# Kernel optimization log

Measured on AMD Instinct MI355X. Metric: run time of the kernel, lower is better.

The kernel has to match this reference:

```python
import jax, jax.numpy as jnp
import numpy as np

D_EMBD = 1024
N_HEADS = 16
D_HEAD = D_EMBD // N_HEADS
BS, T = 2, 2048


def setup_inputs() -> dict:
    key = jax.random.key(0)
    ks = jax.random.split(key, 5)
    s1 = 1.0 / np.sqrt(D_EMBD)
    x = jax.random.normal(ks[0], (BS, T, D_EMBD), dtype=jnp.float32)
    # dense1: Linear(d_embd, 3*d_embd); stored as [in, out] matmul matrix
    W1 = jax.random.uniform(ks[1], (D_EMBD, 3 * D_EMBD), jnp.float32, -s1, s1)
    b1 = jax.random.uniform(ks[2], (3 * D_EMBD,), jnp.float32, -s1, s1)
    # dense2: Linear(d_embd, d_embd)
    W2 = jax.random.uniform(ks[3], (D_EMBD, D_EMBD), jnp.float32, -s1, s1)
    b2 = jax.random.uniform(ks[4], (D_EMBD,), jnp.float32, -s1, s1)
    return {"x": x, "W1": W1, "b1": b1, "W2": W2, "b2": b2}


def reference(x, W1, b1, W2, b2):
    bs, t, d = x.shape
    kqv = x @ W1 + b1                               # [b, t, 3d]
    # torch.chunk order in source: k, q, v
    k, q, v = jnp.split(kqv, 3, axis=-1)
    def heads(z):  # [b, t, (h d)] -> [b, h, t, d]
        return z.reshape(bs, t, N_HEADS, D_HEAD).transpose(0, 2, 1, 3)
    k, q, v = heads(k), heads(q), heads(v)
    scale = 1.0 / np.sqrt(D_HEAD).astype(np.float32)
    attn = jnp.einsum('bhtd,bhsd->bhts', q, k) * scale   # [b, h, t, t]
    causal = jnp.tril(jnp.ones((t, t), dtype=bool))
    attn = jnp.where(causal, attn, -jnp.inf)
    attn = jax.nn.softmax(attn, axis=-1)
    out = jnp.einsum('bhts,bhsd->bhtd', attn, v)         # [b, h, t, d]
    out = out.transpose(0, 2, 1, 3).reshape(bs, t, d)    # [b, t, (h d)]
    return out @ W2 + b2
```

## Files before the change

### kernel.cpp

```cpp
#include <hip/hip_runtime.h>

typedef unsigned short ushort_t;
typedef short bf16x8 __attribute__((ext_vector_type(8)));
typedef float f32x4 __attribute__((ext_vector_type(4)));

__device__ __forceinline__ unsigned f2bf(float f) {
    union { float f; unsigned u; } c; c.f = f;
    unsigned u = c.u;
    u += 0x7FFFu + ((u >> 16) & 1u);
    return u >> 16;
}

__device__ __forceinline__ void async16(const ushort_t* g, ushort_t* l) {
    __builtin_amdgcn_global_load_lds(
        (const __attribute__((address_space(1))) unsigned int*)g,
        (__attribute__((address_space(3))) unsigned int*)l, 16, 0, 0);
}

__global__ __launch_bounds__(256) void prep_kernel(
    const float* __restrict__ x, const float* __restrict__ W1, const float* __restrict__ W2,
    ushort_t* __restrict__ xb, ushort_t* __restrict__ w1t, ushort_t* __restrict__ w2t) {
    __shared__ float tile[64][65];
    const int tid = threadIdx.x;
    const int bid = blockIdx.x;
    if (bid < 2048) {
        const int i = (bid * 256 + tid) * 8;
        const float4 a = *(const float4*)(x + i);
        const float4 b = *(const float4*)(x + i + 4);
        uint4 pk;
        pk.x = f2bf(a.x) | (f2bf(a.y) << 16);
        pk.y = f2bf(a.z) | (f2bf(a.w) << 16);
        pk.z = f2bf(b.x) | (f2bf(b.y) << 16);
        pk.w = f2bf(b.z) | (f2bf(b.w) << 16);
        *(uint4*)(xb + i) = pk;
        return;
    }
    const float* src; ushort_t* dst; int R, C, r0, c0;
    if (bid < 2816) {
        const int t = bid - 2048;
        src = W1; dst = w1t; R = 1024; C = 3072;
        c0 = (t % 48) * 64; r0 = (t / 48) * 64;
    } else {
        const int t = bid - 2816;
        src = W2; dst = w2t; R = 1024; C = 1024;
        c0 = (t & 15) * 64; r0 = (t >> 4) * 64;
    }
    const int rr = tid >> 4, cc = (tid & 15) * 4;
#pragma unroll
    for (int i = 0; i < 4; ++i) {
        const float4 v = *(const float4*)(src + (size_t)(r0 + rr + 16 * i) * C + c0 + cc);
        tile[rr + 16 * i][cc]     = v.x;
        tile[rr + 16 * i][cc + 1] = v.y;
        tile[rr + 16 * i][cc + 2] = v.z;
        tile[rr + 16 * i][cc + 3] = v.w;
    }
    __syncthreads();
#pragma unroll
    for (int i = 0; i < 4; ++i) {
        const int orow = rr + 16 * i;
        uint2 pk;
        pk.x = f2bf(tile[cc][orow])     | (f2bf(tile[cc + 1][orow]) << 16);
        pk.y = f2bf(tile[cc + 2][orow]) | (f2bf(tile[cc + 3][orow]) << 16);
        *(uint2*)(dst + (size_t)(c0 + orow) * R + r0 + cc) = pk;
    }
}

__device__ __forceinline__ void gemm_core_128(const ushort_t* __restrict__ A,
                                              const ushort_t* __restrict__ B,
                                              int m0, int n0,
                                              ushort_t* As, ushort_t* Bs,
                                              f32x4 acc[4][4], int tid) {
    const int w = tid >> 6, lane = tid & 63, quad = lane >> 4, l16 = lane & 15;
    const int wrow = (w >> 1) * 64, wcol = (w & 1) * 64;
    const ushort_t* Ab = A + (size_t)m0 * 1024;
    const ushort_t* Bb = B + (size_t)n0 * 1024;
    for (int kt = 0; kt < 32; ++kt) {
        const int k0 = kt * 32;
#pragma unroll
        for (int c = 0; c < 2; ++c) {
            const int e = c * 2048 + tid * 8;
            const int row = e >> 5, col = e & 31;
            async16(Ab + (size_t)row * 1024 + k0 + col, As + e);
            async16(Bb + (size_t)row * 1024 + k0 + col, Bs + e);
        }
        __syncthreads();
        bf16x8 af[4], bfr[4];
#pragma unroll
        for (int i = 0; i < 4; ++i) {
            af[i]  = *(const bf16x8*)(As + (wrow + i * 16 + l16) * 32 + quad * 8);
            bfr[i] = *(const bf16x8*)(Bs + (wcol + i * 16 + l16) * 32 + quad * 8);
        }
#pragma unroll
        for (int mi = 0; mi < 4; ++mi)
#pragma unroll
            for (int ni = 0; ni < 4; ++ni)
                acc[mi][ni] = __builtin_amdgcn_mfma_f32_16x16x32_bf16(
                    af[mi], bfr[ni], acc[mi][ni], 0, 0, 0);
        __syncthreads();
    }
}

__global__ __launch_bounds__(256) void gemm_qkv_kernel(
    const ushort_t* __restrict__ xb, const ushort_t* __restrict__ w1t,
    const float* __restrict__ b1,
    ushort_t* __restrict__ kb, ushort_t* __restrict__ qb, ushort_t* __restrict__ vb) {
    __shared__ __attribute__((aligned(16))) ushort_t As[128 * 32];
    __shared__ __attribute__((aligned(16))) ushort_t Bs[128 * 32];
    const int tid = threadIdx.x;
    const int m0 = blockIdx.y * 128, n0 = blockIdx.x * 128;
    f32x4 acc[4][4];
    const f32x4 z4 = {0.f, 0.f, 0.f, 0.f};
#pragma unroll
    for (int i = 0; i < 4; ++i)
#pragma unroll
        for (int j = 0; j < 4; ++j) acc[i][j] = z4;
    gemm_core_128(xb, w1t, m0, n0, As, Bs, acc, tid);

    const int w = tid >> 6, lane = tid & 63, quad = lane >> 4, l16 = lane & 15;
    const int wrow = (w >> 1) * 64, wcol = (w & 1) * 64;
    const int chunk = n0 >> 10;
#pragma unroll
    for (int mi = 0; mi < 4; ++mi) {
#pragma unroll
        for (int ni = 0; ni < 4; ++ni) {
            const int cg = n0 + wcol + ni * 16 + l16;
            const float bias = b1[cg];
            const int hc = cg & 1023;
            const int h = hc >> 6, d = hc & 63;
#pragma unroll
            for (int r = 0; r < 4; ++r) {
                const int rg = m0 + wrow + mi * 16 + quad * 4 + r;
                const int bb = rg >> 11, tt = rg & 2047;
                const int bh = bb * 16 + h;
                const float v = acc[mi][ni][r] + bias;
                if (chunk == 0)
                    kb[((size_t)bh * 2048 + tt) * 64 + d] = (ushort_t)f2bf(v);
                else if (chunk == 1)
                    qb[((size_t)bh * 2048 + tt) * 64 + d] = (ushort_t)f2bf(v * 0.1803368801f);
                else
                    vb[((size_t)bh * 64 + d) * 2048 + tt] = (ushort_t)f2bf(v);
            }
        }
    }
}

__global__ __launch_bounds__(256) void attn_kernel(
    const ushort_t* __restrict__ qb, const ushort_t* __restrict__ kb,
    const ushort_t* __restrict__ vb, ushort_t* __restrict__ aout) {
    __shared__ __attribute__((aligned(16))) ushort_t Ks[2][64][72];
    __shared__ __attribute__((aligned(16))) ushort_t Vs[2][64][72];
    __shared__ __attribute__((aligned(16))) ushort_t Ps[4][16][72];

    const int tid = threadIdx.x;
    const int w = tid >> 6, lane = tid & 63, quad = lane >> 4, l16 = lane & 15;
    const int bh = blockIdx.x;
    const int qt = (int)gridDim.y - 1 - (int)blockIdx.y;
    const int q0 = qt * 64;
    const float NEG_INF = -__builtin_inff();

    const ushort_t* Q = qb + (size_t)bh * (2048 * 64);
    const ushort_t* K = kb + (size_t)bh * (2048 * 64);
    const ushort_t* V = vb + (size_t)bh * (64 * 2048);

    const int srow = tid >> 2, scol = (tid & 3) * 16;

    {
        const uint4* src = (const uint4*)(Q + (size_t)(q0 + srow) * 64 + scol);
        *(uint4*)&Ks[0][srow][scol] = src[0];
        *(uint4*)&Ks[0][srow][scol + 8] = src[1];
    }
    const bf16x8 aq0 = *(const bf16x8*)&Ks[0][w * 16 + l16][quad * 8];
    const bf16x8 aq1 = *(const bf16x8*)&Ks[0][w * 16 + l16][quad * 8 + 32];

    uint4 kr0, kr1, vr0, vr1;
    {
        const uint4* kp = (const uint4*)(K + (size_t)srow * 64 + scol);
        kr0 = kp[0]; kr1 = kp[1];
        const uint4* vp = (const uint4*)(V + (size_t)srow * 2048 + scol);
        vr0 = vp[0]; vr1 = vp[1];
    }

    float m_i[4], l_i[4];
    f32x4 o[4];
    const f32x4 z4 = {0.f, 0.f, 0.f, 0.f};
#pragma unroll
    for (int r = 0; r < 4; ++r) { m_i[r] = NEG_INF; l_i[r] = 0.f; }
#pragma unroll
    for (int d = 0; d < 4; ++d) o[d] = z4;

    for (int kt = 0; kt <= qt; ++kt) {
        const int cur = kt & 1;
        *(uint4*)&Ks[cur][srow][scol]     = kr0;
        *(uint4*)&Ks[cur][srow][scol + 8] = kr1;
        *(uint4*)&Vs[cur][srow][scol]     = vr0;
        *(uint4*)&Vs[cur][srow][scol + 8] = vr1;
        __syncthreads();
        if (kt < qt) {
            const uint4* kp = (const uint4*)(K + (size_t)((kt + 1) * 64 + srow) * 64 + scol);
            kr0 = kp[0]; kr1 = kp[1];
            const uint4* vp = (const uint4*)(V + (size_t)srow * 2048 + (kt + 1) * 64 + scol);
            vr0 = vp[0]; vr1 = vp[1];
        }

        f32x4 s[4];
#pragma unroll
        for (int ni = 0; ni < 4; ++ni) s[ni] = z4;
#pragma unroll
        for (int ni = 0; ni < 4; ++ni) {
            const bf16x8 bk0 = *(const bf16x8*)&Ks[cur][ni * 16 + l16][quad * 8];
            const bf16x8 bk1 = *(const bf16x8*)&Ks[cur][ni * 16 + l16][quad * 8 + 32];
            s[ni] = __builtin_amdgcn_mfma_f32_16x16x32_bf16(aq0, bk0, s[ni], 0, 0, 0);
            s[ni] = __builtin_amdgcn_mfma_f32_16x16x32_bf16(aq1, bk1, s[ni], 0, 0, 0);
        }
        if (kt == qt) {
#pragma unroll
            for (int ni = 0; ni < 4; ++ni) {
                const int sg = ni * 16 + l16;
#pragma unroll
                for (int r = 0; r < 4; ++r) {
                    const int qg = w * 16 + quad * 4 + r;
                    if (sg > qg) s[ni][r] = NEG_INF;
                }
            }
        }
        float p[4][4], alpha[4];
#pragma unroll
        for (int r = 0; r < 4; ++r) {
            float rm = fmaxf(fmaxf(s[0][r], s[1][r]), fmaxf(s[2][r], s[3][r]));
            rm = fmaxf(rm, __shfl_xor(rm, 1));
            rm = fmaxf(rm, __shfl_xor(rm, 2));
            rm = fmaxf(rm, __shfl_xor(rm, 4));
            rm = fmaxf(rm, __shfl_xor(rm, 8));
            const float mn = fmaxf(m_i[r], rm);
            alpha[r] = __builtin_amdgcn_exp2f(m_i[r] - mn);
            m_i[r] = mn;
            float rs = 0.f;
#pragma unroll
            for (int ni = 0; ni < 4; ++ni) {
                p[ni][r] = __builtin_amdgcn_exp2f(s[ni][r] - mn);
                rs += p[ni][r];
            }
            rs += __shfl_xor(rs, 1);
            rs += __shfl_xor(rs, 2);
            rs += __shfl_xor(rs, 4);
            rs += __shfl_xor(rs, 8);
            l_i[r] = l_i[r] * alpha[r] + rs;
        }
#pragma unroll
        for (int d = 0; d < 4; ++d)
#pragma unroll
            for (int r = 0; r < 4; ++r) o[d][r] *= alpha[r];

#pragma unroll
        for (int ni = 0; ni < 4; ++ni)
#pragma unroll
            for (int r = 0; r < 4; ++r)
                Ps[w][quad * 4 + r][ni * 16 + l16] = (ushort_t)f2bf(p[ni][r]);
        const bf16x8 ap0 = *(const bf16x8*)&Ps[w][l16][quad * 8];
        const bf16x8 ap1 = *(const bf16x8*)&Ps[w][l16][quad * 8 + 32];
#pragma unroll
        for (int d = 0; d < 4; ++d) {
            const bf16x8 bv0 = *(const bf16x8*)&Vs[cur][d * 16 + l16][quad * 8];
            const bf16x8 bv1 = *(const bf16x8*)&Vs[cur][d * 16 + l16][quad * 8 + 32];
            o[d] = __builtin_amdgcn_mfma_f32_16x16x32_bf16(ap0, bv0, o[d], 0, 0, 0);
            o[d] = __builtin_amdgcn_mfma_f32_16x16x32_bf16(ap1, bv1, o[d], 0, 0, 0);
        }
    }
    const int b = bh >> 4, h = bh & 15;
#pragma unroll
    for (int r = 0; r < 4; ++r) {
        const float inv = 1.0f / l_i[r];
        const int tg = q0 + w * 16 + quad * 4 + r;
#pragma unroll
        for (int d = 0; d < 4; ++d) {
            const int cg = h * 64 + d * 16 + l16;
            aout[(size_t)(b * 2048 + tg) * 1024 + cg] = (ushort_t)f2bf(o[d][r] * inv);
        }
    }
}

__global__ __launch_bounds__(256) void gemm_out_kernel(
    const ushort_t* __restrict__ ab, const ushort_t* __restrict__ w2t,
    const float* __restrict__ b2, float* __restrict__ out) {
    __shared__ __attribute__((aligned(16))) ushort_t As[128 * 32];
    __shared__ __attribute__((aligned(16))) ushort_t Bs[128 * 32];
    const int tid = threadIdx.x;
    const int m0 = blockIdx.y * 128, n0 = blockIdx.x * 128;
    f32x4 acc[4][4];
    const f32x4 z4 = {0.f, 0.f, 0.f, 0.f};
#pragma unroll
    for (int i = 0; i < 4; ++i)
#pragma unroll
        for (int j = 0; j < 4; ++j) acc[i][j] = z4;
    gemm_core_128(ab, w2t, m0, n0, As, Bs, acc, tid);

    const int w = tid >> 6, lane = tid & 63, quad = lane >> 4, l16 = lane & 15;
    const int wrow = (w >> 1) * 64, wcol = (w & 1) * 64;
#pragma unroll
    for (int mi = 0; mi < 4; ++mi) {
#pragma unroll
        for (int ni = 0; ni < 4; ++ni) {
            const int cg = n0 + wcol + ni * 16 + l16;
            const float bias = b2[cg];
#pragma unroll
            for (int r = 0; r < 4; ++r) {
                const int rg = m0 + wrow + mi * 16 + quad * 4 + r;
                out[(size_t)rg * 1024 + cg] = acc[mi][ni][r] + bias;
            }
        }
    }
}

extern "C" void kernel_launch(void* const* d_in, const int* in_sizes, int n_in,
                              void* d_out, int out_size, void* d_ws, size_t ws_size,
                              hipStream_t stream) {
    const float* x  = (const float*)d_in[0];
    const float* W1 = (const float*)d_in[1];
    const float* b1 = (const float*)d_in[2];
    const float* W2 = (const float*)d_in[3];
    const float* b2 = (const float*)d_in[4];
    float* out = (float*)d_out;

    char* ws = (char*)d_ws;
    const size_t MB = 1024 * 1024;
    ushort_t* xb  = (ushort_t*)(ws);
    ushort_t* w1t = (ushort_t*)(ws + 8 * MB);
    ushort_t* w2t = (ushort_t*)(ws + 14 * MB);
    ushort_t* kb  = (ushort_t*)(ws + 16 * MB);
    ushort_t* qb  = (ushort_t*)(ws + 24 * MB);
    ushort_t* vb  = (ushort_t*)(ws + 32 * MB);
    ushort_t* ao  = (ushort_t*)(ws + 40 * MB);

    prep_kernel<<<3072, 256, 0, stream>>>(x, W1, W2, xb, w1t, w2t);
    gemm_qkv_kernel<<<dim3(24, 32), 256, 0, stream>>>(xb, w1t, b1, kb, qb, vb);
    attn_kernel<<<dim3(32, 32), 256, 0, stream>>>(qb, kb, vb, ao);
    gemm_out_kernel<<<dim3(8, 32), 256, 0, stream>>>(ao, w2t, b2, out);
}
```

Baseline: 205.1 us.

## Restructure attention to 128-row tiles with transposed S and register-resident P

The attention kernel now gives each block a 128-query tile, with 32 rows per wave. Query fragments load straight from global memory. S is computed transposed, so each lane holds whole columns, and P is packed in registers as truncated bf16 for 16x16x16 MFMAs against V, which removes the LDS round-trip for P. Waves skip key tiles that lie fully above the causal diagonal, and the q-tile order is interleaved so heavy and light tiles mix. The output GEMM switches to 128x64 tiles with its own inline loop, doubling the block count. Truncating P instead of rounding adds a small precision risk.

```diff
diff --git a/kernel.cpp b/kernel.cpp
--- a/kernel.cpp
+++ b/kernel.cpp
@@ -2,6 +2,7 @@
 
 typedef unsigned short ushort_t;
 typedef short bf16x8 __attribute__((ext_vector_type(8)));
+typedef short bf16x4 __attribute__((ext_vector_type(4)));
 typedef float f32x4 __attribute__((ext_vector_type(4)));
 
 __device__ __forceinline__ unsigned f2bf(float f) {
@@ -9,6 +10,11 @@
     unsigned u = c.u;
     u += 0x7FFFu + ((u >> 16) & 1u);
     return u >> 16;
+}
+
+__device__ __forceinline__ unsigned pack_trunc(float a, float b) {
+    union { float f; unsigned u; } ca, cb; ca.f = a; cb.f = b;
+    return (ca.u >> 16) | (cb.u & 0xFFFF0000u);
 }
 
 __device__ __forceinline__ void async16(const ushort_t* g, ushort_t* l) {
@@ -149,28 +155,29 @@
     const ushort_t* __restrict__ vb, ushort_t* __restrict__ aout) {
     __shared__ __attribute__((aligned(16))) ushort_t Ks[2][64][72];
     __shared__ __attribute__((aligned(16))) ushort_t Vs[2][64][72];
-    __shared__ __attribute__((aligned(16))) ushort_t Ps[4][16][72];
 
     const int tid = threadIdx.x;
     const int w = tid >> 6, lane = tid & 63, quad = lane >> 4, l16 = lane & 15;
     const int bh = blockIdx.x;
-    const int qt = (int)gridDim.y - 1 - (int)blockIdx.y;
-    const int q0 = qt * 64;
+    const int yy = (int)blockIdx.y;
+    const int qtile = (yy < 8) ? (15 - yy) : (yy - 8);
+    const int q0 = qtile * 128;
+    const int ktmax = 2 * qtile + 1;
+    const int q0w = q0 + w * 32;
     const float NEG_INF = -__builtin_inff();
 
     const ushort_t* Q = qb + (size_t)bh * (2048 * 64);
     const ushort_t* K = kb + (size_t)bh * (2048 * 64);
     const ushort_t* V = vb + (size_t)bh * (64 * 2048);
 
+    bf16x8 aq[2][2];
+#pragma unroll
+    for (int u = 0; u < 2; ++u)
+#pragma unroll
+        for (int kh = 0; kh < 2; ++kh)
+            aq[u][kh] = *(const bf16x8*)(Q + (size_t)(q0w + u * 16 + l16) * 64 + kh * 32 + quad * 8);
+
     const int srow = tid >> 2, scol = (tid & 3) * 16;
-
-    {
-        const uint4* src = (const uint4*)(Q + (size_t)(q0 + srow) * 64 + scol);
-        *(uint4*)&Ks[0][srow][scol] = src[0];
-        *(uint4*)&Ks[0][srow][scol + 8] = src[1];
-    }
-    const bf16x8 aq0 = *(const bf16x8*)&Ks[0][w * 16 + l16][quad * 8];
-    const bf16x8 aq1 = *(const bf16x8*)&Ks[0][w * 16 + l16][quad * 8 + 32];
 
     uint4 kr0, kr1, vr0, vr1;
     {
@@ -180,101 +187,111 @@
         vr0 = vp[0]; vr1 = vp[1];
     }
 
-    float m_i[4], l_i[4];
-    f32x4 o[4];
+    float m_i[2] = {NEG_INF, NEG_INF}, l_i[2] = {0.f, 0.f};
+    f32x4 o[2][4];
     const f32x4 z4 = {0.f, 0.f, 0.f, 0.f};
 #pragma unroll
-    for (int r = 0; r < 4; ++r) { m_i[r] = NEG_INF; l_i[r] = 0.f; }
-#pragma unroll
-    for (int d = 0; d < 4; ++d) o[d] = z4;
-
-    for (int kt = 0; kt <= qt; ++kt) {
+    for (int u = 0; u < 2; ++u)
+#pragma unroll
+        for (int d = 0; d < 4; ++d) o[u][d] = z4;
+
+    for (int kt = 0; kt <= ktmax; ++kt) {
         const int cur = kt & 1;
         *(uint4*)&Ks[cur][srow][scol]     = kr0;
         *(uint4*)&Ks[cur][srow][scol + 8] = kr1;
         *(uint4*)&Vs[cur][srow][scol]     = vr0;
         *(uint4*)&Vs[cur][srow][scol + 8] = vr1;
         __syncthreads();
-        if (kt < qt) {
+        if (kt < ktmax) {
             const uint4* kp = (const uint4*)(K + (size_t)((kt + 1) * 64 + srow) * 64 + scol);
             kr0 = kp[0]; kr1 = kp[1];
             const uint4* vp = (const uint4*)(V + (size_t)srow * 2048 + (kt + 1) * 64 + scol);
             vr0 = vp[0]; vr1 = vp[1];
         }
-
-        f32x4 s[4];
-#pragma unroll
-        for (int ni = 0; ni < 4; ++ni) s[ni] = z4;
-#pragma unroll
-        for (int ni = 0; ni < 4; ++ni) {
-            const bf16x8 bk0 = *(const bf16x8*)&Ks[cur][ni * 16 + l16][quad * 8];
-            const bf16x8 bk1 = *(const bf16x8*)&Ks[cur][ni * 16 + l16][quad * 8 + 32];
-            s[ni] = __builtin_amdgcn_mfma_f32_16x16x32_bf16(aq0, bk0, s[ni], 0, 0, 0);
-            s[ni] = __builtin_amdgcn_mfma_f32_16x16x32_bf16(aq1, bk1, s[ni], 0, 0, 0);
-        }
-        if (kt == qt) {
+        if (kt * 64 >= q0w + 32) continue;
+
+        bf16x8 af[4][2];
+#pragma unroll
+        for (int ni = 0; ni < 4; ++ni)
+#pragma unroll
+            for (int kh = 0; kh < 2; ++kh)
+                af[ni][kh] = *(const bf16x8*)&Ks[cur][ni * 16 + l16][kh * 32 + quad * 8];
+        f32x4 st[2][4];
+#pragma unroll
+        for (int u = 0; u < 2; ++u)
 #pragma unroll
             for (int ni = 0; ni < 4; ++ni) {
-                const int sg = ni * 16 + l16;
+                f32x4 acc = z4;
+                acc = __builtin_amdgcn_mfma_f32_16x16x32_bf16(af[ni][0], aq[u][0], acc, 0, 0, 0);
+                acc = __builtin_amdgcn_mfma_f32_16x16x32_bf16(af[ni][1], aq[u][1], acc, 0, 0, 0);
+                st[u][ni] = acc;
+            }
+        if (kt >= 2 * qtile) {
+#pragma unroll
+            for (int u = 0; u < 2; ++u)
+#pragma unroll
+                for (int ni = 0; ni < 4; ++ni)
+#pragma unroll
+                    for (int r = 0; r < 4; ++r) {
+                        const int s = kt * 64 + ni * 16 + quad * 4 + r;
+                        const int q = q0w + u * 16 + l16;
+                        if (s > q) st[u][ni][r] = NEG_INF;
+                    }
+        }
+        bf16x4 ph[2][4];
+#pragma unroll
+        for (int u = 0; u < 2; ++u) {
+            float mx = st[u][0][0];
+#pragma unroll
+            for (int ni = 0; ni < 4; ++ni)
+#pragma unroll
+                for (int r = 0; r < 4; ++r) mx = fmaxf(mx, st[u][ni][r]);
+            mx = fmaxf(mx, __shfl_xor(mx, 16));
+            mx = fmaxf(mx, __shfl_xor(mx, 32));
+            const float mn = fmaxf(m_i[u], mx);
+            const float alpha = __builtin_amdgcn_exp2f(m_i[u] - mn);
+            m_i[u] = mn;
+            float p[4][4], rs = 0.f;
+#pragma unroll
+            for (int ni = 0; ni < 4; ++ni)
 #pragma unroll
                 for (int r = 0; r < 4; ++r) {
-                    const int qg = w * 16 + quad * 4 + r;
-                    if (sg > qg) s[ni][r] = NEG_INF;
+                    p[ni][r] = __builtin_amdgcn_exp2f(st[u][ni][r] - mn);
+                    rs += p[ni][r];
                 }
-            }
-        }
-        float p[4][4], alpha[4];
-#pragma unroll
-        for (int r = 0; r < 4; ++r) {
-            float rm = fmaxf(fmaxf(s[0][r], s[1][r]), fmaxf(s[2][r], s[3][r]));
-            rm = fmaxf(rm, __shfl_xor(rm, 1));
-            rm = fmaxf(rm, __shfl_xor(rm, 2));
-            rm = fmaxf(rm, __shfl_xor(rm, 4));
-            rm = fmaxf(rm, __shfl_xor(rm, 8));
-            const float mn = fmaxf(m_i[r], rm);
-            alpha[r] = __builtin_amdgcn_exp2f(m_i[r] - mn);
-            m_i[r] = mn;
-            float rs = 0.f;
+            rs += __shfl_xor(rs, 16);
+            rs += __shfl_xor(rs, 32);
+            l_i[u] = l_i[u] * alpha + rs;
+#pragma unroll
+            for (int d = 0; d < 4; ++d) o[u][d] *= alpha;
 #pragma unroll
             for (int ni = 0; ni < 4; ++ni) {
-                p[ni][r] = __builtin_amdgcn_exp2f(s[ni][r] - mn);
-                rs += p[ni][r];
-            }
-            rs += __shfl_xor(rs, 1);
-            rs += __shfl_xor(rs, 2);
-            rs += __shfl_xor(rs, 4);
-            rs += __shfl_xor(rs, 8);
-            l_i[r] = l_i[r] * alpha[r] + rs;
-        }
-#pragma unroll
-        for (int d = 0; d < 4; ++d)
-#pragma unroll
-            for (int r = 0; r < 4; ++r) o[d][r] *= alpha[r];
-
+                union { bf16x4 v; uint2 uu; } pk;
+                pk.uu.x = pack_trunc(p[ni][0], p[ni][1]);
+                pk.uu.y = pack_trunc(p[ni][2], p[ni][3]);
+                ph[u][ni] = pk.v;
+            }
+        }
 #pragma unroll
         for (int ni = 0; ni < 4; ++ni)
 #pragma unroll
-            for (int r = 0; r < 4; ++r)
-                Ps[w][quad * 4 + r][ni * 16 + l16] = (ushort_t)f2bf(p[ni][r]);
-        const bf16x8 ap0 = *(const bf16x8*)&Ps[w][l16][quad * 8];
-        const bf16x8 ap1 = *(const bf16x8*)&Ps[w][l16][quad * 8 + 32];
-#pragma unroll
-        for (int d = 0; d < 4; ++d) {
-            const bf16x8 bv0 = *(const bf16x8*)&Vs[cur][d * 16 + l16][quad * 8];
-            const bf16x8 bv1 = *(const bf16x8*)&Vs[cur][d * 16 + l16][quad * 8 + 32];
-            o[d] = __builtin_amdgcn_mfma_f32_16x16x32_bf16(ap0, bv0, o[d], 0, 0, 0);
-            o[d] = __builtin_amdgcn_mfma_f32_16x16x32_bf16(ap1, bv1, o[d], 0, 0, 0);
-        }
+            for (int dt = 0; dt < 4; ++dt) {
+                const bf16x4 av = *(const bf16x4*)&Vs[cur][dt * 16 + l16][ni * 16 + quad * 4];
+                o[0][dt] = __builtin_amdgcn_mfma_f32_16x16x16bf16_1k(av, ph[0][ni], o[0][dt], 0, 0, 0);
+                o[1][dt] = __builtin_amdgcn_mfma_f32_16x16x16bf16_1k(av, ph[1][ni], o[1][dt], 0, 0, 0);
+            }
     }
     const int b = bh >> 4, h = bh & 15;
 #pragma unroll
-    for (int r = 0; r < 4; ++r) {
-        const float inv = 1.0f / l_i[r];
-        const int tg = q0 + w * 16 + quad * 4 + r;
-#pragma unroll
-        for (int d = 0; d < 4; ++d) {
-            const int cg = h * 64 + d * 16 + l16;
-            aout[(size_t)(b * 2048 + tg) * 1024 + cg] = (ushort_t)f2bf(o[d][r] * inv);
+    for (int u = 0; u < 2; ++u) {
+        const float inv = 1.0f / l_i[u];
+        const int q = q0w + u * 16 + l16;
+#pragma unroll
+        for (int dt = 0; dt < 4; ++dt) {
+            uint2 pk;
+            pk.x = f2bf(o[u][dt][0] * inv) | (f2bf(o[u][dt][1] * inv) << 16);
+            pk.y = f2bf(o[u][dt][2] * inv) | (f2bf(o[u][dt][3] * inv) << 16);
+            *(uint2*)&aout[(size_t)(b * 2048 + q) * 1024 + h * 64 + dt * 16 + quad * 4] = pk;
         }
     }
 }
@@ -283,28 +300,52 @@
     const ushort_t* __restrict__ ab, const ushort_t* __restrict__ w2t,
     const float* __restrict__ b2, float* __restrict__ out) {
     __shared__ __attribute__((aligned(16))) ushort_t As[128 * 32];
-    __shared__ __attribute__((aligned(16))) ushort_t Bs[128 * 32];
+    __shared__ __attribute__((aligned(16))) ushort_t Bs[64 * 32];
     const int tid = threadIdx.x;
-    const int m0 = blockIdx.y * 128, n0 = blockIdx.x * 128;
-    f32x4 acc[4][4];
+    const int w = tid >> 6, lane = tid & 63, quad = lane >> 4, l16 = lane & 15;
+    const int n0 = blockIdx.x * 64, m0 = blockIdx.y * 128;
+    f32x4 acc[2][4];
     const f32x4 z4 = {0.f, 0.f, 0.f, 0.f};
 #pragma unroll
-    for (int i = 0; i < 4; ++i)
+    for (int i = 0; i < 2; ++i)
 #pragma unroll
         for (int j = 0; j < 4; ++j) acc[i][j] = z4;
-    gemm_core_128(ab, w2t, m0, n0, As, Bs, acc, tid);
-
-    const int w = tid >> 6, lane = tid & 63, quad = lane >> 4, l16 = lane & 15;
-    const int wrow = (w >> 1) * 64, wcol = (w & 1) * 64;
-#pragma unroll
-    for (int mi = 0; mi < 4; ++mi) {
+    const ushort_t* Ab = ab + (size_t)m0 * 1024;
+    const ushort_t* Bb = w2t + (size_t)n0 * 1024;
+    for (int kt = 0; kt < 32; ++kt) {
+        const int k0 = kt * 32;
+        {
+            const int e = tid * 8;
+            async16(Ab + (size_t)(e >> 5) * 1024 + k0 + (e & 31), As + e);
+            const int e2 = 2048 + e;
+            async16(Ab + (size_t)(e2 >> 5) * 1024 + k0 + (e2 & 31), As + e2);
+            async16(Bb + (size_t)(e >> 5) * 1024 + k0 + (e & 31), Bs + e);
+        }
+        __syncthreads();
+        bf16x8 af[2], bfr[4];
+#pragma unroll
+        for (int mi = 0; mi < 2; ++mi)
+            af[mi] = *(const bf16x8*)(As + (w * 32 + mi * 16 + l16) * 32 + quad * 8);
+#pragma unroll
+        for (int ni = 0; ni < 4; ++ni)
+            bfr[ni] = *(const bf16x8*)(Bs + (ni * 16 + l16) * 32 + quad * 8);
+#pragma unroll
+        for (int mi = 0; mi < 2; ++mi)
+#pragma unroll
+            for (int ni = 0; ni < 4; ++ni)
+                acc[mi][ni] = __builtin_amdgcn_mfma_f32_16x16x32_bf16(
+                    af[mi], bfr[ni], acc[mi][ni], 0, 0, 0);
+        __syncthreads();
+    }
+#pragma unroll
+    for (int mi = 0; mi < 2; ++mi) {
 #pragma unroll
         for (int ni = 0; ni < 4; ++ni) {
-            const int cg = n0 + wcol + ni * 16 + l16;
+            const int cg = n0 + ni * 16 + l16;
             const float bias = b2[cg];
 #pragma unroll
             for (int r = 0; r < 4; ++r) {
-                const int rg = m0 + wrow + mi * 16 + quad * 4 + r;
+                const int rg = m0 + w * 32 + mi * 16 + quad * 4 + r;
                 out[(size_t)rg * 1024 + cg] = acc[mi][ni][r] + bias;
             }
         }
@@ -333,6 +374,6 @@
 
     prep_kernel<<<3072, 256, 0, stream>>>(x, W1, W2, xb, w1t, w2t);
     gemm_qkv_kernel<<<dim3(24, 32), 256, 0, stream>>>(xb, w1t, b1, kb, qb, vb);
-    attn_kernel<<<dim3(32, 32), 256, 0, stream>>>(qb, kb, vb, ao);
-    gemm_out_kernel<<<dim3(8, 32), 256, 0, stream>>>(ao, w2t, b2, out);
-}
+    attn_kernel<<<dim3(32, 16), 256, 0, stream>>>(qb, kb, vb, ao);
+    gemm_out_kernel<<<dim3(16, 32), 256, 0, stream>>>(ao, w2t, b2, out);
+}
```

Result: faster. 190.7 us (-7.0%).
